# Optimization experiments

Hardware: AMD Instinct MI355X
Metric: run time of the kernel (lower is better)

The kernel has to match this reference:

```python
import jax, jax.numpy as jnp
import numpy as np

D_MODEL = 1024
NUM_HEADS = 16
D_HEAD = D_MODEL // NUM_HEADS


def setup_inputs() -> dict:
    key = jax.random.key(0)
    ks = jax.random.split(key, 5)
    b, n = 4, 2048
    x = jax.random.normal(ks[0], (b, n, D_MODEL), dtype=jnp.float32)
    s = 1.0 / np.sqrt(D_MODEL)
    w_qkv = jax.random.normal(ks[1], (D_MODEL, 3 * D_MODEL), dtype=jnp.float32) * s
    b_qkv = jax.random.normal(ks[2], (3 * D_MODEL,), dtype=jnp.float32) * 0.01
    w_out = jax.random.normal(ks[3], (D_MODEL, D_MODEL), dtype=jnp.float32) * s
    b_out = jax.random.normal(ks[4], (D_MODEL,), dtype=jnp.float32) * 0.01
    return {"x": x, "w_qkv": w_qkv, "b_qkv": b_qkv, "w_out": w_out, "b_out": b_out}


def reference(x, w_qkv, b_qkv, w_out, b_out):
    b, n, _ = x.shape
    h, d = NUM_HEADS, D_HEAD
    scale = d ** -0.5
    qkv = x @ w_qkv + b_qkv                       # [b, n, 3*d_model]
    # split as (qkv, h, d) on the feature axis, matching 'b n (qkv h d)'
    qkv = qkv.reshape(b, n, 3, h, d).transpose(2, 0, 3, 1, 4)  # [3, b, h, n, d]
    q, k, v = qkv[0], qkv[1], qkv[2]
    dots = jnp.einsum('bhid,bhjd->bhij', q, k) * scale
    causal = jnp.tril(jnp.ones((n, n), dtype=bool))
    dots = jnp.where(causal[None, None], dots, -jnp.inf)
    attn = jax.nn.softmax(dots, axis=-1)
    out = jnp.einsum('bhij,bhjd->bhid', attn, v)
    out = out.transpose(0, 2, 1, 3).reshape(b, n, h * d)
    return out @ w_out + b_out
```

## Files before the change

### kernel.cpp

```cpp
#include <hip/hip_runtime.h>
#include <hip/hip_bf16.h>
#include <stdint.h>

typedef unsigned short u16;
typedef __attribute__((ext_vector_type(8))) short bf16x8;
typedef __attribute__((ext_vector_type(4))) float f32x4;
typedef __attribute__((ext_vector_type(16))) float f32x16;
typedef __attribute__((ext_vector_type(4))) short s16x4;
typedef __attribute__((ext_vector_type(2))) unsigned u32x2;

#define SEQ   2048
#define BATCH 4

#define MFMA16(a,b,c) __builtin_amdgcn_mfma_f32_16x16x32_bf16(a,b,c,0,0,0)
#define MFMA32(a,b,c) __builtin_amdgcn_mfma_f32_32x32x16_bf16(a,b,c,0,0,0)
#define EXP2F __builtin_amdgcn_exp2f

__device__ __forceinline__ u16 f2bf(float f) {
  union { float f; uint32_t u; } c{f};
  uint32_t r = c.u + 0x7fffu + ((c.u >> 16) & 1u);
  return (u16)(r >> 16);
}

__device__ __forceinline__ void gll16(const void* g, void* l) {
  __builtin_amdgcn_global_load_lds((const __attribute__((address_space(1))) void*)g,
                                   (__attribute__((address_space(3))) void*)l,
                                   16, 0, 0);
}

__device__ __forceinline__ void plswap(uint32_t &a, uint32_t &b) {
  u32x2 r = __builtin_amdgcn_permlane32_swap(a, b, false, false);
  a = r[0]; b = r[1];
}
__device__ __forceinline__ float xhalf_max(float v) {
  union { float f; uint32_t u; } c{v};
  u32x2 r = __builtin_amdgcn_permlane32_swap(c.u, c.u, false, false);
  union { uint32_t u; float f; } x{r[0]}, y{r[1]};
  return fmaxf(x.f, y.f);
}
__device__ __forceinline__ float xhalf_add(float v) {
  union { float f; uint32_t u; } c{v};
  u32x2 r = __builtin_amdgcn_permlane32_swap(c.u, c.u, false, false);
  union { uint32_t u; float f; } x{r[0]}, y{r[1]};
  return x.f + y.f;
}

__global__ __launch_bounds__(256) void k_cvt(const float* __restrict__ in,
                                             u16* __restrict__ out) {
  int i = (blockIdx.x * 256 + threadIdx.x) * 8;
  float4 a = *(const float4*)(in + i);
  float4 b = *(const float4*)(in + i + 4);
  union { u16 u[8]; bf16x8 v; } r;
  r.u[0] = f2bf(a.x); r.u[1] = f2bf(a.y); r.u[2] = f2bf(a.z); r.u[3] = f2bf(a.w);
  r.u[4] = f2bf(b.x); r.u[5] = f2bf(b.y); r.u[6] = f2bf(b.z); r.u[7] = f2bf(b.w);
  *(bf16x8*)(out + i) = r.v;
}

__global__ __launch_bounds__(256) void k_cvtT(const float* __restrict__ in,
                                              u16* __restrict__ out, int K, int N) {
  __shared__ float tl[32][33];
  int tx = threadIdx.x & 31, ty = threadIdx.x >> 5;
  int c0 = blockIdx.x * 32, r0 = blockIdx.y * 32;
#pragma unroll
  for (int j = 0; j < 32; j += 8)
    tl[ty + j][tx] = in[(size_t)(r0 + ty + j) * N + c0 + tx];
  __syncthreads();
#pragma unroll
  for (int j = 0; j < 32; j += 8)
    out[(size_t)(c0 + ty + j) * K + r0 + tx] = f2bf(tl[tx][ty + j]);
}

#define SBAR  asm volatile("s_barrier" ::: "memory")
#define LGKM0 asm volatile("s_waitcnt lgkmcnt(0)" ::: "memory")
#define VM2   asm volatile("s_waitcnt vmcnt(2)" ::: "memory")
#define VM0   asm volatile("s_waitcnt vmcnt(0)" ::: "memory")
#define FEN   asm volatile("" ::: "memory")

template<int OUT_F32>
__global__ __launch_bounds__(512, 2) void k_gemm256(const u16* __restrict__ A,
                                                    const u16* __restrict__ BT,
                                                    const float* __restrict__ bias,
                                                    void* __restrict__ Cv,
                                                    int N, int K, int NT, int TN) {
  __shared__ alignas(16) char LDS[98304];
  const int t = threadIdx.x;
  const int l = t & 63, w = t >> 6;
  const int wm = w >> 2, wn = w & 3;
  const int lr = l & 15, lg = l >> 4;

  const int nwg = gridDim.x;
  const int cpx = nwg >> 3;
  const int sb = (blockIdx.x & 7) * cpx + (blockIdx.x >> 3);
  const int brow = (sb / TN) * 256, bcol = (sb % TN) * 128;

  auto stageA = [&](int c, int h, int tt) {
#pragma unroll
    for (int i = 0; i < 2; i++) {
      int s = t + i * 512;
      int r = s >> 3, cg = s & 7;
      int grow = brow + (r >> 6) * 128 + h * 64 + (r & 63);
      int gk = tt * 64 + ((cg ^ (r & 7)) * 8);
      gll16(A + (size_t)grow * K + gk, LDS + c * 49152 + h * 16384 + s * 16);
    }
  };
  auto stageB = [&](int c, int tt) {
#pragma unroll
    for (int i = 0; i < 2; i++) {
      int s = t + i * 512;
      int r = s >> 3, cg = s & 7;
      int grow = bcol + r;
      int gk = tt * 64 + ((cg ^ (r & 7)) * 8);
      gll16(BT + (size_t)grow * K + gk, LDS + c * 49152 + 32768 + s * 16);
    }
  };

  f32x4 acc[8][2] = {};
  bf16x8 afr[4], bfr[2];

#define READ_A(c, h, ks)                                                       \
  {                                                                            \
    const char* baseA = LDS + (c) * 49152 + (h) * 16384 + (wm * 64) * 128;     \
    _Pragma("unroll") for (int mi = 0; mi < 4; mi++)                           \
      afr[mi] = *(const bf16x8*)(baseA + (mi * 16 + lr) * 128 +                \
                                 ((((ks) * 4 + lg) ^ (lr & 7)) * 16));         \
  }
#define READ_B(c, ks)                                                          \
  {                                                                            \
    const char* baseB = LDS + (c) * 49152 + 32768 + (wn * 32) * 128;           \
    _Pragma("unroll") for (int ni = 0; ni < 2; ni++)                           \
      bfr[ni] = *(const bf16x8*)(baseB + (ni * 16 + lr) * 128 +                \
                                 ((((ks) * 4 + lg) ^ (lr & 7)) * 16));         \
  }
#define DO_MFMA(H)                                                             \
  {                                                                            \
    __builtin_amdgcn_s_setprio(1);                                             \
    _Pragma("unroll") for (int mi = 0; mi < 4; mi++)                           \
      _Pragma("unroll") for (int ni = 0; ni < 2; ni++)                         \
        acc[(H)*4 + mi][ni] = MFMA16(afr[mi], bfr[ni], acc[(H)*4 + mi][ni]);   \
    __builtin_amdgcn_s_setprio(0);                                             \
  }

  stageA(0, 0, 0); FEN;
  stageB(0, 0);    FEN;
  stageA(0, 1, 0); FEN;
  VM2; SBAR;

  for (int tt = 0; tt < NT; tt++) {
    const int c = tt & 1;
    if (tt + 1 < NT) { stageA(c ^ 1, 0, tt + 1); FEN; }
    READ_A(c, 0, 0); READ_B(c, 0);
    DO_MFMA(0);
    if (tt + 1 < NT) { VM2; } else { VM0; }
    LGKM0; SBAR;
    if (tt + 1 < NT) { stageB(c ^ 1, tt + 1); FEN; }
    READ_A(c, 1, 0);
    DO_MFMA(1);
    if (tt + 1 < NT) { stageA(c ^ 1, 1, tt + 1); FEN; }
    READ_A(c, 1, 1); READ_B(c, 1);
    DO_MFMA(1);
    READ_A(c, 0, 1);
    DO_MFMA(0);
    VM2;
    LGKM0; SBAR;
  }

  const int r0 = brow + wm * 128 + lg * 4;
  const int c0 = bcol + wn * 32 + lr;
#pragma unroll
  for (int ni = 0; ni < 2; ni++) {
    float bv = bias[c0 + ni * 16];
#pragma unroll
    for (int mig = 0; mig < 8; mig++) {
      const int row = r0 + mig * 16;
#pragma unroll
      for (int r = 0; r < 4; r++) {
        float v = acc[mig][ni][r] + bv;
        size_t off = (size_t)(row + r) * N + c0 + ni * 16;
        if (OUT_F32) ((float*)Cv)[off] = v;
        else         ((u16*)Cv)[off]   = f2bf(v);
      }
    }
  }
}
#undef READ_A
#undef READ_B
#undef DO_MFMA

__global__ __launch_bounds__(256) void k_trV(const u16* __restrict__ qkv,
                                             u16* __restrict__ vT) {
  __shared__ u16 s[32][33];
  int tx = threadIdx.x & 31, ty = threadIdx.x >> 5;
  int n0 = blockIdx.x * 32, d0 = blockIdx.y * 32, bh = blockIdx.z;
  int b = bh >> 4, h = bh & 15;
#pragma unroll
  for (int j = 0; j < 32; j += 8)
    s[ty + j][tx] = qkv[(size_t)(b * SEQ + n0 + ty + j) * 3072 + 2048 + h * 64 + d0 + tx];
  __syncthreads();
#pragma unroll
  for (int j = 0; j < 32; j += 8)
    vT[(size_t)(bh * 64 + d0 + ty + j) * SEQ + n0 + tx] = s[tx][ty + j];
}

__global__ __launch_bounds__(256) void k_attn(const u16* __restrict__ qkv,
                                              const u16* __restrict__ vT,
                                              u16* __restrict__ outp) {
  __shared__ alignas(16) char SB[2][16384];
  const int t = threadIdx.x, l = t & 63, w = t >> 6;
  const int hi = l >> 5, q = l & 31;
  const int qp = blockIdx.x, h = blockIdx.y, b = blockIdx.z;
  const int bh = b * 16 + h;
  const int srow = t >> 3;
  const int csw = ((t & 7) * 16) ^ ((srow & 7) << 4);
  const int swz = (q & 7) << 4;
  const float SC = 0.18033688011112042f;

  auto STAGE = [&](char* buf, int kv0) {
    char* lK = buf + w * 1024;
    char* lV = buf + 8192 + w * 1024;
    gll16(qkv + (size_t)(b * SEQ + kv0 + srow) * 3072 + 1024 + h * 64 + (csw >> 1), lK);
    gll16(qkv + (size_t)(b * SEQ + kv0 + srow + 32) * 3072 + 1024 + h * 64 + (csw >> 1), lK + 4096);
    gll16(vT + (size_t)(bh * 64 + srow) * SEQ + kv0 + (csw >> 1), lV);
    gll16(vT + (size_t)(bh * 64 + srow + 32) * SEQ + kv0 + (csw >> 1), lV + 4096);
  };

  for (int tsel = 0; tsel < 2; tsel++) {
    const int qt = tsel ? (15 - qp) : qp;
    const int qr0 = qt * 128 + w * 32;
    const int qg = qr0 + q;
    bf16x8 qf[4];
#pragma unroll
    for (int c = 0; c < 4; c++)
      qf[c] = *(const bf16x8*)(qkv + (size_t)(b * SEQ + qg) * 3072 + h * 64 + c * 16 + hi * 8);
    f32x16 o0 = {}, o1 = {}, lv = {};
    float m_run = -1e30f;
    const int nkv = 2 * qt + 2;

    STAGE(SB[0], 0);
    for (int j = 0; j < nkv; j++) {
      const int kv0 = j * 64;
      __syncthreads();
      if (j + 1 < nkv) STAGE(SB[(j + 1) & 1], kv0 + 64);
      const char* Kb = SB[j & 1];
      const char* Vb = Kb + 8192;

      if (kv0 <= qr0 + 31) {
        f32x16 st0 = {}, st1 = {};
        __builtin_amdgcn_s_setprio(1);
#pragma unroll
        for (int c = 0; c < 4; c++) {
          const int cb = c * 32 + hi * 16;
          bf16x8 k0 = *(const bf16x8*)(Kb + q * 128 + (cb ^ swz));
          bf16x8 k1 = *(const bf16x8*)(Kb + (32 + q) * 128 + (cb ^ swz));
          st0 = MFMA32(k0, qf[c], st0);
          st1 = MFMA32(k1, qf[c], st1);
        }
        __builtin_amdgcn_s_setprio(0);
        if (kv0 + 63 > qr0) {
#pragma unroll
          for (int r = 0; r < 16; r++) {
            const int krow = (r & 3) + 8 * (r >> 2) + 4 * hi;
            if (kv0 + krow > qg)      st0[r] = -1e30f;
            if (kv0 + 32 + krow > qg) st1[r] = -1e30f;
          }
        }
        float tmx[16];
#pragma unroll
        for (int r = 0; r < 16; r++) tmx[r] = fmaxf(st0[r], st1[r]);
        float v0 = fmaxf(fmaxf(tmx[0], tmx[1]), tmx[2]);
        float v1 = fmaxf(fmaxf(tmx[3], tmx[4]), tmx[5]);
        float v2 = fmaxf(fmaxf(tmx[6], tmx[7]), tmx[8]);
        float v3 = fmaxf(fmaxf(tmx[9], tmx[10]), tmx[11]);
        float v4 = fmaxf(fmaxf(tmx[12], tmx[13]), tmx[14]);
        float v5 = fmaxf(fmaxf(v0, v1), tmx[15]);
        float v6 = fmaxf(fmaxf(v2, v3), v4);
        float v7 = fmaxf(v5, v6);
        const float vs = xhalf_max(v7) * SC;
        if (__any(vs > m_run + 8.0f)) {
          float mnew = fmaxf(m_run, vs);
          float corr = EXP2F(m_run - mnew);
          m_run = mnew;
#pragma unroll
          for (int r = 0; r < 16; r++) { o0[r] *= corr; o1[r] *= corr; lv[r] *= corr; }
        }
        f32x16 e0 = st0 * SC - m_run;
        f32x16 e1 = st1 * SC - m_run;
        f32x16 p0, p1;
#pragma unroll
        for (int r = 0; r < 16; r++) { p0[r] = EXP2F(e0[r]); p1[r] = EXP2F(e1[r]); }
        lv += p0 + p1;
#pragma unroll
        for (int khb = 0; khb < 2; khb++) {
          uint32_t pk[8];
#pragma unroll
          for (int ii = 0; ii < 8; ii++) {
            float lo = khb ? p1[2 * ii] : p0[2 * ii];
            float hf = khb ? p1[2 * ii + 1] : p0[2 * ii + 1];
            asm("v_cvt_pk_bf16_f32 %0, %1, %2" : "=v"(pk[ii]) : "v"(lo), "v"(hf));
          }
          plswap(pk[0], pk[2]); plswap(pk[1], pk[3]);
          plswap(pk[4], pk[6]); plswap(pk[5], pk[7]);
          union { uint32_t u[4]; bf16x8 v; } be, bo;
          be.u[0] = pk[0]; be.u[1] = pk[1]; be.u[2] = pk[2]; be.u[3] = pk[3];
          bo.u[0] = pk[4]; bo.u[1] = pk[5]; bo.u[2] = pk[6]; bo.u[3] = pk[7];
          __builtin_amdgcn_s_setprio(1);
#pragma unroll
          for (int kti = 0; kti < 2; kti++) {
            const int cb = (khb * 2 + kti) * 32 + hi * 16;
            bf16x8 vv0 = *(const bf16x8*)(Vb + q * 128 + (cb ^ swz));
            bf16x8 vv1 = *(const bf16x8*)(Vb + (32 + q) * 128 + (cb ^ swz));
            bf16x8 pb = kti ? bo.v : be.v;
            o0 = MFMA32(vv0, pb, o0);
            o1 = MFMA32(vv1, pb, o1);
          }
          __builtin_amdgcn_s_setprio(0);
        }
      }
    }
    __syncthreads();
    float ls = ((lv[0] + lv[1]) + (lv[2] + lv[3])) + ((lv[4] + lv[5]) + (lv[6] + lv[7]))
             + ((lv[8] + lv[9]) + (lv[10] + lv[11])) + ((lv[12] + lv[13]) + (lv[14] + lv[15]));
    ls = xhalf_add(ls);
    const float invl = 1.0f / ls;
#pragma unroll
    for (int dh = 0; dh < 2; dh++)
#pragma unroll
      for (int jq = 0; jq < 4; jq++) {
        union { u16 u[4]; s16x4 v; } pk4;
#pragma unroll
        for (int r = 0; r < 4; r++)
          pk4.u[r] = f2bf((dh ? o1[4 * jq + r] : o0[4 * jq + r]) * invl);
        *(s16x4*)(outp + (size_t)(b * SEQ + qg) * 1024 + h * 64 + dh * 32 + jq * 8 + hi * 4) = pk4.v;
      }
  }
}

extern "C" void kernel_launch(void* const* d_in, const int* in_sizes, int n_in,
                              void* d_out, int out_size, void* d_ws, size_t ws_size,
                              hipStream_t stream) {
  const float* x     = (const float*)d_in[0];
  const float* w_qkv = (const float*)d_in[1];
  const float* b_qkv = (const float*)d_in[2];
  const float* w_out = (const float*)d_in[3];
  const float* b_out = (const float*)d_in[4];

  char* ws = (char*)d_ws;
  u16* xbf   = (u16*)(ws);
  u16* wqkvT = (u16*)(ws + (16u << 20));
  u16* woutT = (u16*)(ws + (22u << 20));
  u16* qkvb  = (u16*)(ws + (24u << 20));
  u16* vTb   = (u16*)(ws + (72u << 20));

  k_cvt <<<4096, 256, 0, stream>>>(x, xbf);
  k_cvtT<<<dim3(96, 32), 256, 0, stream>>>(w_qkv, wqkvT, 1024, 3072);
  k_cvtT<<<dim3(32, 32), 256, 0, stream>>>(w_out, woutT, 1024, 1024);
  k_gemm256<0><<<768, 512, 0, stream>>>(xbf, wqkvT, b_qkv, qkvb, 3072, 1024, 16, 24);
  k_trV <<<dim3(64, 2, 64), 256, 0, stream>>>(qkvb, vTb);
  k_attn<<<dim3(8, 16, 4), 256, 0, stream>>>(qkvb, vTb, xbf);
  k_gemm256<1><<<256, 512, 0, stream>>>(xbf, woutT, b_out, d_out, 1024, 1024, 16, 8);
}
```

Before: 179.5 us.

## Process adjacent query tile pair concurrently with 512-thread attention blocks sharing K/V

Each attention block previously looped sequentially over two balanced query tiles (qp and 15-qp) with 4 waves. It now launches 8 waves that handle two adjacent 128-row query tiles at once and share one K/V staging pass, with each thread loading half as much per stage. Load balance now comes from reversing the tile-pair index for batches 2-3 instead of the complementary-tile pairing, so individual blocks do uneven amounts of work. The waves of the lower tile sit idle at barriers during the last KV steps, and occupancy is bounded by launch_bounds(512,4).

```diff
diff --git a/kernel.cpp b/kernel.cpp
--- a/kernel.cpp
+++ b/kernel.cpp
@@ -201,137 +201,136 @@
     vT[(size_t)(bh * 64 + d0 + ty + j) * SEQ + n0 + tx] = s[tx][ty + j];
 }
 
-__global__ __launch_bounds__(256) void k_attn(const u16* __restrict__ qkv,
-                                              const u16* __restrict__ vT,
-                                              u16* __restrict__ outp) {
+__global__ __launch_bounds__(512, 4) void k_attn(const u16* __restrict__ qkv,
+                                                 const u16* __restrict__ vT,
+                                                 u16* __restrict__ outp) {
   __shared__ alignas(16) char SB[2][16384];
   const int t = threadIdx.x, l = t & 63, w = t >> 6;
   const int hi = l >> 5, q = l & 31;
-  const int qp = blockIdx.x, h = blockIdx.y, b = blockIdx.z;
+  const int gp = blockIdx.x, h = blockIdx.y, b = blockIdx.z;
   const int bh = b * 16 + h;
+  const int g_eff = (b >= 2) ? (7 - gp) : gp;
+  const int qt = 2 * g_eff + (w >> 2);
+  const int wq = w & 3;
+  const int qr0 = qt * 128 + wq * 32;
+  const int qg = qr0 + q;
+  const int nkv_mine = 2 * qt + 2;
+  const int nkv_max  = 4 * g_eff + 4;
+
   const int srow = t >> 3;
   const int csw = ((t & 7) * 16) ^ ((srow & 7) << 4);
   const int swz = (q & 7) << 4;
   const float SC = 0.18033688011112042f;
 
   auto STAGE = [&](char* buf, int kv0) {
-    char* lK = buf + w * 1024;
-    char* lV = buf + 8192 + w * 1024;
-    gll16(qkv + (size_t)(b * SEQ + kv0 + srow) * 3072 + 1024 + h * 64 + (csw >> 1), lK);
-    gll16(qkv + (size_t)(b * SEQ + kv0 + srow + 32) * 3072 + 1024 + h * 64 + (csw >> 1), lK + 4096);
-    gll16(vT + (size_t)(bh * 64 + srow) * SEQ + kv0 + (csw >> 1), lV);
-    gll16(vT + (size_t)(bh * 64 + srow + 32) * SEQ + kv0 + (csw >> 1), lV + 4096);
+    gll16(qkv + (size_t)(b * SEQ + kv0 + srow) * 3072 + 1024 + h * 64 + (csw >> 1),
+          buf + w * 1024);
+    gll16(vT + (size_t)(bh * 64 + srow) * SEQ + kv0 + (csw >> 1),
+          buf + 8192 + w * 1024);
   };
 
-  for (int tsel = 0; tsel < 2; tsel++) {
-    const int qt = tsel ? (15 - qp) : qp;
-    const int qr0 = qt * 128 + w * 32;
-    const int qg = qr0 + q;
-    bf16x8 qf[4];
-#pragma unroll
-    for (int c = 0; c < 4; c++)
-      qf[c] = *(const bf16x8*)(qkv + (size_t)(b * SEQ + qg) * 3072 + h * 64 + c * 16 + hi * 8);
-    f32x16 o0 = {}, o1 = {}, lv = {};
-    float m_run = -1e30f;
-    const int nkv = 2 * qt + 2;
-
-    STAGE(SB[0], 0);
-    for (int j = 0; j < nkv; j++) {
-      const int kv0 = j * 64;
-      __syncthreads();
-      if (j + 1 < nkv) STAGE(SB[(j + 1) & 1], kv0 + 64);
-      const char* Kb = SB[j & 1];
-      const char* Vb = Kb + 8192;
-
-      if (kv0 <= qr0 + 31) {
-        f32x16 st0 = {}, st1 = {};
+  bf16x8 qf[4];
+#pragma unroll
+  for (int c = 0; c < 4; c++)
+    qf[c] = *(const bf16x8*)(qkv + (size_t)(b * SEQ + qg) * 3072 + h * 64 + c * 16 + hi * 8);
+  f32x16 o0 = {}, o1 = {}, lv = {};
+  float m_run = -1e30f;
+
+  STAGE(SB[0], 0);
+  for (int j = 0; j < nkv_max; j++) {
+    const int kv0 = j * 64;
+    __syncthreads();
+    if (j + 1 < nkv_max) STAGE(SB[(j + 1) & 1], kv0 + 64);
+    const char* Kb = SB[j & 1];
+    const char* Vb = Kb + 8192;
+
+    if (j < nkv_mine && kv0 <= qr0 + 31) {
+      f32x16 st0 = {}, st1 = {};
+      __builtin_amdgcn_s_setprio(1);
+#pragma unroll
+      for (int c = 0; c < 4; c++) {
+        const int cb = c * 32 + hi * 16;
+        bf16x8 k0 = *(const bf16x8*)(Kb + q * 128 + (cb ^ swz));
+        bf16x8 k1 = *(const bf16x8*)(Kb + (32 + q) * 128 + (cb ^ swz));
+        st0 = MFMA32(k0, qf[c], st0);
+        st1 = MFMA32(k1, qf[c], st1);
+      }
+      __builtin_amdgcn_s_setprio(0);
+      if (kv0 + 63 > qr0) {
+#pragma unroll
+        for (int r = 0; r < 16; r++) {
+          const int krow = (r & 3) + 8 * (r >> 2) + 4 * hi;
+          if (kv0 + krow > qg)      st0[r] = -1e30f;
+          if (kv0 + 32 + krow > qg) st1[r] = -1e30f;
+        }
+      }
+      float tmx[16];
+#pragma unroll
+      for (int r = 0; r < 16; r++) tmx[r] = fmaxf(st0[r], st1[r]);
+      float v0 = fmaxf(fmaxf(tmx[0], tmx[1]), tmx[2]);
+      float v1 = fmaxf(fmaxf(tmx[3], tmx[4]), tmx[5]);
+      float v2 = fmaxf(fmaxf(tmx[6], tmx[7]), tmx[8]);
+      float v3 = fmaxf(fmaxf(tmx[9], tmx[10]), tmx[11]);
+      float v4 = fmaxf(fmaxf(tmx[12], tmx[13]), tmx[14]);
+      float v5 = fmaxf(fmaxf(v0, v1), tmx[15]);
+      float v6 = fmaxf(fmaxf(v2, v3), v4);
+      float v7 = fmaxf(v5, v6);
+      const float vs = xhalf_max(v7) * SC;
+      if (__any(vs > m_run + 8.0f)) {
+        float mnew = fmaxf(m_run, vs);
+        float corr = EXP2F(m_run - mnew);
+        m_run = mnew;
+#pragma unroll
+        for (int r = 0; r < 16; r++) { o0[r] *= corr; o1[r] *= corr; lv[r] *= corr; }
+      }
+      f32x16 e0 = st0 * SC - m_run;
+      f32x16 e1 = st1 * SC - m_run;
+      f32x16 p0, p1;
+#pragma unroll
+      for (int r = 0; r < 16; r++) { p0[r] = EXP2F(e0[r]); p1[r] = EXP2F(e1[r]); }
+      lv += p0 + p1;
+#pragma unroll
+      for (int khb = 0; khb < 2; khb++) {
+        uint32_t pk[8];
+#pragma unroll
+        for (int ii = 0; ii < 8; ii++) {
+          float lo = khb ? p1[2 * ii] : p0[2 * ii];
+          float hf = khb ? p1[2 * ii + 1] : p0[2 * ii + 1];
+          asm("v_cvt_pk_bf16_f32 %0, %1, %2" : "=v"(pk[ii]) : "v"(lo), "v"(hf));
+        }
+        plswap(pk[0], pk[2]); plswap(pk[1], pk[3]);
+        plswap(pk[4], pk[6]); plswap(pk[5], pk[7]);
+        union { uint32_t u[4]; bf16x8 v; } be, bo;
+        be.u[0] = pk[0]; be.u[1] = pk[1]; be.u[2] = pk[2]; be.u[3] = pk[3];
+        bo.u[0] = pk[4]; bo.u[1] = pk[5]; bo.u[2] = pk[6]; bo.u[3] = pk[7];
         __builtin_amdgcn_s_setprio(1);
 #pragma unroll
-        for (int c = 0; c < 4; c++) {
-          const int cb = c * 32 + hi * 16;
-          bf16x8 k0 = *(const bf16x8*)(Kb + q * 128 + (cb ^ swz));
-          bf16x8 k1 = *(const bf16x8*)(Kb + (32 + q) * 128 + (cb ^ swz));
-          st0 = MFMA32(k0, qf[c], st0);
-          st1 = MFMA32(k1, qf[c], st1);
+        for (int kti = 0; kti < 2; kti++) {
+          const int cb = (khb * 2 + kti) * 32 + hi * 16;
+          bf16x8 vv0 = *(const bf16x8*)(Vb + q * 128 + (cb ^ swz));
+          bf16x8 vv1 = *(const bf16x8*)(Vb + (32 + q) * 128 + (cb ^ swz));
+          bf16x8 pb = kti ? bo.v : be.v;
+          o0 = MFMA32(vv0, pb, o0);
+          o1 = MFMA32(vv1, pb, o1);
         }
         __builtin_amdgcn_s_setprio(0);
-        if (kv0 + 63 > qr0) {
-#pragma unroll
-          for (int r = 0; r < 16; r++) {
-            const int krow = (r & 3) + 8 * (r >> 2) + 4 * hi;
-            if (kv0 + krow > qg)      st0[r] = -1e30f;
-            if (kv0 + 32 + krow > qg) st1[r] = -1e30f;
-          }
-        }
-        float tmx[16];
-#pragma unroll
-        for (int r = 0; r < 16; r++) tmx[r] = fmaxf(st0[r], st1[r]);
-        float v0 = fmaxf(fmaxf(tmx[0], tmx[1]), tmx[2]);
-        float v1 = fmaxf(fmaxf(tmx[3], tmx[4]), tmx[5]);
-        float v2 = fmaxf(fmaxf(tmx[6], tmx[7]), tmx[8]);
-        float v3 = fmaxf(fmaxf(tmx[9], tmx[10]), tmx[11]);
-        float v4 = fmaxf(fmaxf(tmx[12], tmx[13]), tmx[14]);
-        float v5 = fmaxf(fmaxf(v0, v1), tmx[15]);
-        float v6 = fmaxf(fmaxf(v2, v3), v4);
-        float v7 = fmaxf(v5, v6);
-        const float vs = xhalf_max(v7) * SC;
-        if (__any(vs > m_run + 8.0f)) {
-          float mnew = fmaxf(m_run, vs);
-          float corr = EXP2F(m_run - mnew);
-          m_run = mnew;
-#pragma unroll
-          for (int r = 0; r < 16; r++) { o0[r] *= corr; o1[r] *= corr; lv[r] *= corr; }
-        }
-        f32x16 e0 = st0 * SC - m_run;
-        f32x16 e1 = st1 * SC - m_run;
-        f32x16 p0, p1;
-#pragma unroll
-        for (int r = 0; r < 16; r++) { p0[r] = EXP2F(e0[r]); p1[r] = EXP2F(e1[r]); }
-        lv += p0 + p1;
-#pragma unroll
-        for (int khb = 0; khb < 2; khb++) {
-          uint32_t pk[8];
-#pragma unroll
-          for (int ii = 0; ii < 8; ii++) {
-            float lo = khb ? p1[2 * ii] : p0[2 * ii];
-            float hf = khb ? p1[2 * ii + 1] : p0[2 * ii + 1];
-            asm("v_cvt_pk_bf16_f32 %0, %1, %2" : "=v"(pk[ii]) : "v"(lo), "v"(hf));
-          }
-          plswap(pk[0], pk[2]); plswap(pk[1], pk[3]);
-          plswap(pk[4], pk[6]); plswap(pk[5], pk[7]);
-          union { uint32_t u[4]; bf16x8 v; } be, bo;
-          be.u[0] = pk[0]; be.u[1] = pk[1]; be.u[2] = pk[2]; be.u[3] = pk[3];
-          bo.u[0] = pk[4]; bo.u[1] = pk[5]; bo.u[2] = pk[6]; bo.u[3] = pk[7];
-          __builtin_amdgcn_s_setprio(1);
-#pragma unroll
-          for (int kti = 0; kti < 2; kti++) {
-            const int cb = (khb * 2 + kti) * 32 + hi * 16;
-            bf16x8 vv0 = *(const bf16x8*)(Vb + q * 128 + (cb ^ swz));
-            bf16x8 vv1 = *(const bf16x8*)(Vb + (32 + q) * 128 + (cb ^ swz));
-            bf16x8 pb = kti ? bo.v : be.v;
-            o0 = MFMA32(vv0, pb, o0);
-            o1 = MFMA32(vv1, pb, o1);
-          }
-          __builtin_amdgcn_s_setprio(0);
-        }
-      }
-    }
-    __syncthreads();
-    float ls = ((lv[0] + lv[1]) + (lv[2] + lv[3])) + ((lv[4] + lv[5]) + (lv[6] + lv[7]))
-             + ((lv[8] + lv[9]) + (lv[10] + lv[11])) + ((lv[12] + lv[13]) + (lv[14] + lv[15]));
-    ls = xhalf_add(ls);
-    const float invl = 1.0f / ls;
-#pragma unroll
-    for (int dh = 0; dh < 2; dh++)
-#pragma unroll
-      for (int jq = 0; jq < 4; jq++) {
-        union { u16 u[4]; s16x4 v; } pk4;
-#pragma unroll
-        for (int r = 0; r < 4; r++)
-          pk4.u[r] = f2bf((dh ? o1[4 * jq + r] : o0[4 * jq + r]) * invl);
-        *(s16x4*)(outp + (size_t)(b * SEQ + qg) * 1024 + h * 64 + dh * 32 + jq * 8 + hi * 4) = pk4.v;
-      }
-  }
+      }
+    }
+  }
+  float ls = ((lv[0] + lv[1]) + (lv[2] + lv[3])) + ((lv[4] + lv[5]) + (lv[6] + lv[7]))
+           + ((lv[8] + lv[9]) + (lv[10] + lv[11])) + ((lv[12] + lv[13]) + (lv[14] + lv[15]));
+  ls = xhalf_add(ls);
+  const float invl = 1.0f / ls;
+#pragma unroll
+  for (int dh = 0; dh < 2; dh++)
+#pragma unroll
+    for (int jq = 0; jq < 4; jq++) {
+      union { u16 u[4]; s16x4 v; } pk4;
+#pragma unroll
+      for (int r = 0; r < 4; r++)
+        pk4.u[r] = f2bf((dh ? o1[4 * jq + r] : o0[4 * jq + r]) * invl);
+      *(s16x4*)(outp + (size_t)(b * SEQ + qg) * 1024 + h * 64 + dh * 32 + jq * 8 + hi * 4) = pk4.v;
+    }
 }
 
 extern "C" void kernel_launch(void* const* d_in, const int* in_sizes, int n_in,
@@ -355,6 +354,6 @@
   k_cvtT<<<dim3(32, 32), 256, 0, stream>>>(w_out, woutT, 1024, 1024);
   k_gemm256<0><<<768, 512, 0, stream>>>(xbf, wqkvT, b_qkv, qkvb, 3072, 1024, 16, 24);
   k_trV <<<dim3(64, 2, 64), 256, 0, stream>>>(qkvb, vTb);
-  k_attn<<<dim3(8, 16, 4), 256, 0, stream>>>(qkvb, vTb, xbf);
+  k_attn<<<dim3(8, 16, 4), 512, 0, stream>>>(qkvb, vTb, xbf);
   k_gemm256<1><<<256, 512, 0, stream>>>(xbf, woutT, b_out, d_out, 1024, 1024, 16, 8);
 }
```

Measured after the change: 201.3 us. 12.2% more time.
